# Kernel optimization log

Hardware: AMD Instinct MI355X
Metric: run time of the kernel (lower is better)

The kernel has to match this reference:

```python
import jax, jax.numpy as jnp
import numpy as np

B, T, C = 4, 2048, 1024
H = 16
D = C // H  # head_dim = 64


def setup_inputs() -> dict:
    key = jax.random.key(0)
    k1, k2, k3 = jax.random.split(key, 3)
    x = jax.random.normal(k1, (B, T, C), dtype=jnp.float32)
    w_qkv = jax.random.normal(k2, (3 * C, C), dtype=jnp.float32) * (1.0 / np.sqrt(C))
    w_proj = jax.random.normal(k3, (C, C), dtype=jnp.float32) * (1.0 / np.sqrt(C))
    return {"x": x, "w_qkv": w_qkv, "w_proj": w_proj}


def reference(x, w_qkv, w_proj):
    Bx, Tx, Cx = x.shape
    qkv = jnp.einsum('btc,fc->btf', x, w_qkv)  # [B,T,3C]
    q, k, v = jnp.split(qkv, 3, axis=-1)
    # [B,H,T,D]
    q = q.reshape(Bx, Tx, H, D).transpose(0, 2, 1, 3)
    k = k.reshape(Bx, Tx, H, D).transpose(0, 2, 1, 3)
    v = v.reshape(Bx, Tx, H, D).transpose(0, 2, 1, 3)
    scale = 1.0 / np.sqrt(D)
    scores = jnp.einsum('bhqd,bhkd->bhqk', q, k) * scale
    causal = jnp.tril(jnp.ones((Tx, Tx), dtype=bool))
    scores = jnp.where(causal, scores, jnp.finfo(scores.dtype).min)
    attn = jax.nn.softmax(scores, axis=-1)
    out = jnp.einsum('bhqk,bhkd->bhqd', attn, v)  # [B,H,T,D]
    out = out.transpose(0, 2, 1, 3).reshape(Bx, Tx, Cx)
    return jnp.einsum('btc,oc->bto', out, w_proj)
```

## Files before the change

### kernel.cpp

```cpp
#include <hip/hip_runtime.h>
#include <hip/hip_bf16.h>
#include <stdint.h>

#define Bx 4
#define Tx 2048
#define Cx 1024
#define Hx 16
#define Dx 64
#define Mx (Bx*Tx)

typedef __bf16 bf16x8 __attribute__((ext_vector_type(8)));
typedef float f32x4 __attribute__((ext_vector_type(4)));
typedef unsigned short u16x8 __attribute__((ext_vector_type(8)));

__device__ __forceinline__ unsigned short f2bf(float f) {
  union { float f; unsigned u; } v; v.f = f;
  unsigned r = v.u + 0x7fffu + ((v.u >> 16) & 1u);
  return (unsigned short)(r >> 16);
}

__device__ __forceinline__ unsigned cvt_pk_bf16(float a, float b) {
  unsigned r;
  asm("v_cvt_pk_bf16_f32 %0, %1, %2" : "=v"(r) : "v"(a), "v"(b));
  return r;
}

__global__ void cvt3_kernel(const float* __restrict__ x, const float* __restrict__ wq,
                            const float* __restrict__ wp,
                            unsigned short* __restrict__ xb, unsigned short* __restrict__ wqb,
                            unsigned short* __restrict__ wpb) {
  const int n1 = Bx * Tx * Cx;
  const int n2 = 3 * Cx * Cx;
  int idx = (blockIdx.x * blockDim.x + threadIdx.x) << 3;
  const float* src; unsigned short* dst; int off;
  if (idx < n1)            { src = x;  dst = xb;  off = idx; }
  else if (idx < n1 + n2)  { src = wq; dst = wqb; off = idx - n1; }
  else                     { src = wp; dst = wpb; off = idx - n1 - n2; }
  const float4* p = (const float4*)(src + off);
  float4 a = p[0], b = p[1];
  u16x8 o;
  o[0] = f2bf(a.x); o[1] = f2bf(a.y); o[2] = f2bf(a.z); o[3] = f2bf(a.w);
  o[4] = f2bf(b.x); o[5] = f2bf(b.y); o[6] = f2bf(b.z); o[7] = f2bf(b.w);
  *(u16x8*)(dst + off) = o;
}

#define GLOAD_LDS16(g, l) \
  __builtin_amdgcn_global_load_lds((const __attribute__((address_space(1))) void*)(g), \
                                   (__attribute__((address_space(3))) void*)(l), 16, 0, 0)

template<int OUT_F32>
__global__ __launch_bounds__(512, 1) void gemm8p(const unsigned short* __restrict__ A,
                                                 const unsigned short* __restrict__ Bm,
                                                 void* __restrict__ Cv,
                                                 int M, int N, int K)
{
  __shared__ unsigned short As[3][256 * 64];
  __shared__ unsigned short Bs[3][128 * 64];
  const int tid = threadIdx.x;
  const int wave = tid >> 6, lane = tid & 63;
  const int l15 = lane & 15, l4 = lane >> 4;
  const int wm = wave >> 1, wn = wave & 1;
  const int NB = N >> 7;
  const int cpx = (int)gridDim.x >> 3;
  const int bid = (int)blockIdx.x;
  const int swz = (bid & 7) * cpx + (bid >> 3);
  const int bx = swz % NB, by = swz / NB;
  const int mBase = by << 8, nBase = bx << 7;

  const int srow   = tid >> 3;
  const int schunk = (tid & 7) ^ (srow & 7);
  const unsigned short* aSrc = A  + (size_t)(mBase + srow) * K + (schunk << 3);
  const unsigned short* bSrc = Bm + (size_t)(nBase + srow) * K + (schunk << 3);
  const int dstOff = wave << 9;

  f32x4 acc[4][4];
  #pragma unroll
  for (int i = 0; i < 4; ++i)
    #pragma unroll
    for (int j = 0; j < 4; ++j) { acc[i][j][0]=0.f; acc[i][j][1]=0.f; acc[i][j][2]=0.f; acc[i][j][3]=0.f; }

  const int NT = K >> 6;
  const int s7 = l15 & 7;

#define STG_A(k0, dst, j)  GLOAD_LDS16(aSrc + (size_t)(64*(j))*K + (k0), (dst) + 4096*(j) + dstOff)
#define STG_B(k0, dst, j)  GLOAD_LDS16(bSrc + (size_t)(64*(j))*K + (k0), (dst) + 4096*(j) + dstOff)

  STG_A(0, As[0], 0); STG_A(0, As[0], 1); STG_A(0, As[0], 2); STG_A(0, As[0], 3);
  STG_B(0, Bs[0], 0); STG_B(0, Bs[0], 1);
  STG_A(64, As[1], 0); STG_A(64, As[1], 1); STG_A(64, As[1], 2); STG_A(64, As[1], 3);
  STG_B(64, Bs[1], 0); STG_B(64, Bs[1], 1);

  int bufR = 0;
  for (int t = 0; t < NT; ++t) {
    if (t + 1 < NT) asm volatile("s_waitcnt vmcnt(6)" ::: "memory");
    else            asm volatile("s_waitcnt vmcnt(0)" ::: "memory");
    __builtin_amdgcn_s_barrier();
    asm volatile("" ::: "memory");

    const unsigned short* curA = As[bufR];
    const unsigned short* curB = Bs[bufR];
    int bufS = bufR + 2; if (bufS >= 3) bufS -= 3;
    unsigned short* sA = As[bufS];
    unsigned short* sB = Bs[bufS];
    const bool doStage = (t + 2 < NT);
    const int k2 = (t + 2) << 6;

    if (doStage) { STG_A(k2, sA, 0); STG_A(k2, sA, 1); STG_A(k2, sA, 2); }
    {
      const int ch = l4 ^ s7;
      bf16x8 af[4], bfr[4];
      #pragma unroll
      for (int mi = 0; mi < 4; ++mi)
        af[mi]  = *(const bf16x8*)&curA[((wm << 6) + (mi << 4) + l15) * 64 + (ch << 3)];
      #pragma unroll
      for (int nj = 0; nj < 4; ++nj)
        bfr[nj] = *(const bf16x8*)&curB[((wn << 6) + (nj << 4) + l15) * 64 + (ch << 3)];
      __builtin_amdgcn_s_setprio(1);
      #pragma unroll
      for (int mi = 0; mi < 4; ++mi)
        #pragma unroll
        for (int nj = 0; nj < 4; ++nj)
          acc[mi][nj] = __builtin_amdgcn_mfma_f32_16x16x32_bf16(af[mi], bfr[nj], acc[mi][nj], 0, 0, 0);
      __builtin_amdgcn_s_setprio(0);
    }
    if (doStage) { STG_A(k2, sA, 3); STG_B(k2, sB, 0); STG_B(k2, sB, 1); }
    {
      const int ch = (4 | l4) ^ s7;
      bf16x8 af[4], bfr[4];
      #pragma unroll
      for (int mi = 0; mi < 4; ++mi)
        af[mi]  = *(const bf16x8*)&curA[((wm << 6) + (mi << 4) + l15) * 64 + (ch << 3)];
      #pragma unroll
      for (int nj = 0; nj < 4; ++nj)
        bfr[nj] = *(const bf16x8*)&curB[((wn << 6) + (nj << 4) + l15) * 64 + (ch << 3)];
      __builtin_amdgcn_s_setprio(1);
      #pragma unroll
      for (int mi = 0; mi < 4; ++mi)
        #pragma unroll
        for (int nj = 0; nj < 4; ++nj)
          acc[mi][nj] = __builtin_amdgcn_mfma_f32_16x16x32_bf16(af[mi], bfr[nj], acc[mi][nj], 0, 0, 0);
      __builtin_amdgcn_s_setprio(0);
    }
    asm volatile("" ::: "memory");
    bufR = (bufR == 2) ? 0 : bufR + 1;
  }
#undef STG_A
#undef STG_B

  #pragma unroll
  for (int mi = 0; mi < 4; ++mi)
    #pragma unroll
    for (int nj = 0; nj < 4; ++nj) {
      const int row = mBase + (wm << 6) + (mi << 4) + (l4 << 2);
      const int col = nBase + (wn << 6) + (nj << 4) + l15;
      #pragma unroll
      for (int r = 0; r < 4; ++r) {
        float v = acc[mi][nj][r];
        if (OUT_F32) ((float*)Cv)[(size_t)(row + r) * N + col] = v;
        else ((unsigned short*)Cv)[(size_t)(row + r) * N + col] = f2bf(v);
      }
    }
}

__global__ void vtrans_kernel(const unsigned short* __restrict__ qkv, unsigned short* __restrict__ vt) {
  const int bh = blockIdx.y;
  const int b = bh >> 4, h = bh & 15;
  const int t0 = blockIdx.x << 6;
  __shared__ unsigned short tile[64][65];
  const int tid = threadIdx.x;
  const unsigned short* src = qkv + (size_t)b * Tx * 3072 + 2048 + h * 64;
  for (int e = tid; e < 4096; e += 256) {
    int r = e >> 6, c = e & 63;
    tile[c][r] = src[(size_t)(t0 + r) * 3072 + c];
  }
  __syncthreads();
  unsigned short* dst = vt + (size_t)bh * 64 * Tx + t0;
  for (int e = tid; e < 4096; e += 256) {
    int d = e >> 6, tt = e & 63;
    dst[(size_t)d * Tx + tt] = tile[d][tt];
  }
}

__device__ __forceinline__ void compute_half(
    const unsigned short* __restrict__ Ks, const unsigned short* __restrict__ Vs,
    unsigned short* __restrict__ Plw,
    bf16x8 aq0, bf16x8 aq1, float& m_run, float& rs, f32x4* oacc,
    int qrow0, int kv0, bool diag, int l15, int l4)
{
  const float SC = 0.125f * 1.44269504f;
  f32x4 s[4];
  #pragma unroll
  for (int nt = 0; nt < 4; ++nt) { s[nt][0]=0.f; s[nt][1]=0.f; s[nt][2]=0.f; s[nt][3]=0.f; }
  #pragma unroll
  for (int nt = 0; nt < 4; ++nt) {
    const int r = (nt << 4) + l15, sz = r & 7;
    bf16x8 bk0 = *(const bf16x8*)&Ks[r * 64 + ((l4 ^ sz) << 3)];
    bf16x8 bk1 = *(const bf16x8*)&Ks[r * 64 + (((l4 + 4) ^ sz) << 3)];
    s[nt] = __builtin_amdgcn_mfma_f32_16x16x32_bf16(bk0, aq0, s[nt], 0, 0, 0);
    s[nt] = __builtin_amdgcn_mfma_f32_16x16x32_bf16(bk1, aq1, s[nt], 0, 0, 0);
  }
  if (diag) {
    const int q = qrow0 + l15;
    #pragma unroll
    for (int nt = 0; nt < 4; ++nt) {
      const int kvb = kv0 + (nt << 4) + (l4 << 2);
      #pragma unroll
      for (int r = 0; r < 4; ++r)
        if (kvb + r > q) s[nt][r] = -3.0e38f;
    }
  }
  float pm = fmaxf(fmaxf(fmaxf(s[0][0],s[0][1]),fmaxf(s[0][2],s[0][3])),
                   fmaxf(fmaxf(s[1][0],s[1][1]),fmaxf(s[1][2],s[1][3])));
  pm = fmaxf(pm, fmaxf(fmaxf(fmaxf(s[2][0],s[2][1]),fmaxf(s[2][2],s[2][3])),
                       fmaxf(fmaxf(s[3][0],s[3][1]),fmaxf(s[3][2],s[3][3]))));
  const float DEFER = 44.36142f;
  if (!__all(pm <= m_run + DEFER)) {
    pm = fmaxf(pm, __shfl_xor(pm, 16));
    pm = fmaxf(pm, __shfl_xor(pm, 32));
    const float mnew = fmaxf(m_run, pm);
    const float corr = exp2f((m_run - mnew) * SC);
    rs *= corr;
    float corrT[4];
    #pragma unroll
    for (int r = 0; r < 4; ++r) corrT[r] = __shfl(corr, (l4 << 2) + r);
    #pragma unroll
    for (int nt = 0; nt < 4; ++nt)
      #pragma unroll
      for (int r = 0; r < 4; ++r) oacc[nt][r] *= corrT[r];
    m_run = mnew;
  }
  const float msc = m_run * SC;
  float lsum = 0.f;
  #pragma unroll
  for (int nt = 0; nt < 4; ++nt)
    #pragma unroll
    for (int r = 0; r < 4; ++r) {
      float p = exp2f(__builtin_fmaf(s[nt][r], SC, -msc));
      s[nt][r] = p;
      lsum += p;
    }
  rs += lsum;
  #pragma unroll
  for (int nt = 0; nt < 4; ++nt) {
    uint2 u;
    u.x = cvt_pk_bf16(s[nt][0], s[nt][1]);
    u.y = cvt_pk_bf16(s[nt][2], s[nt][3]);
    *(uint2*)&Plw[l15 * 72 + (nt << 4) + (l4 << 2)] = u;
  }
  asm volatile("s_waitcnt lgkmcnt(0)" ::: "memory");
  __builtin_amdgcn_sched_barrier(0);
  bf16x8 ap0 = *(const bf16x8*)&Plw[l15 * 72 + (l4 << 3)];
  bf16x8 ap1 = *(const bf16x8*)&Plw[l15 * 72 + 32 + (l4 << 3)];
  #pragma unroll
  for (int nt = 0; nt < 4; ++nt) {
    const int r = (nt << 4) + l15, vz = r & 7;
    bf16x8 bv0 = *(const bf16x8*)&Vs[r * 64 + ((l4 ^ vz) << 3)];
    bf16x8 bv1 = *(const bf16x8*)&Vs[r * 64 + (((l4 + 4) ^ vz) << 3)];
    oacc[nt] = __builtin_amdgcn_mfma_f32_16x16x32_bf16(ap0, bv0, oacc[nt], 0, 0, 0);
    oacc[nt] = __builtin_amdgcn_mfma_f32_16x16x32_bf16(ap1, bv1, oacc[nt], 0, 0, 0);
  }
}

__global__ __launch_bounds__(256, 4) void attn_kernel(const unsigned short* __restrict__ qkv,
                                                      const unsigned short* __restrict__ vt,
                                                      unsigned short* __restrict__ aout)
{
  const int id = blockIdx.x;
  const int xcd = id & 7, sblk = id >> 3;
  const int xblk = sblk & 15;
  const int bh = (xcd << 3) + (sblk >> 4);
  const int b = bh >> 4, h = bh & 15;
  const int wave = threadIdx.x >> 6, lane = threadIdx.x & 63;
  const int l15 = lane & 15, l4 = lane >> 4;
  const int qi0 = (xblk << 2) + wave;

  const unsigned short* qp = qkv + (size_t)b * Tx * 3072 + h * 64;
  const unsigned short* kp = qp + 1024;
  const unsigned short* vp = vt + (size_t)bh * 64 * Tx;
  unsigned short* op = aout + (size_t)b * Tx * 1024 + h * 64;

  __shared__ unsigned short Ks[64 * 64];
  __shared__ unsigned short Vs[64 * 64];
  __shared__ unsigned short Pl[4][2][16 * 72];

  const int qiA = qi0, qiB = 127 - qi0;
  const int qrA = qiA << 4, qrB = qiB << 4;
  const int lastA = xblk, lastB = 31 - xblk;

  bf16x8 aqA0 = *(const bf16x8*)&qp[(size_t)(qrA + l15) * 3072 + (l4 << 3)];
  bf16x8 aqA1 = *(const bf16x8*)&qp[(size_t)(qrA + l15) * 3072 + 32 + (l4 << 3)];
  bf16x8 aqB0 = *(const bf16x8*)&qp[(size_t)(qrB + l15) * 3072 + (l4 << 3)];
  bf16x8 aqB1 = *(const bf16x8*)&qp[(size_t)(qrB + l15) * 3072 + 32 + (l4 << 3)];

  float mA = 0.f, rsA = 0.f, mB = 0.f, rsB = 0.f;
  f32x4 oA[4], oB[4];
  #pragma unroll
  for (int nt = 0; nt < 4; ++nt) {
    oA[nt][0]=0.f; oA[nt][1]=0.f; oA[nt][2]=0.f; oA[nt][3]=0.f;
    oB[nt][0]=0.f; oB[nt][1]=0.f; oB[nt][2]=0.f; oB[nt][3]=0.f;
  }

  const int srw = lane >> 3;
  const int sj  = (lane & 7) ^ srw;

  for (int kvt = 0; kvt <= lastB; ++kvt) {
    const int kv0 = kvt << 6;
    {
      const int c0 = wave << 1, c1 = c0 + 1;
      const int r0 = (c0 << 3) + srw, r1 = (c1 << 3) + srw;
      GLOAD_LDS16(kp + (size_t)(kv0 + r0) * 3072 + (sj << 3), Ks + (c0 << 9));
      GLOAD_LDS16(kp + (size_t)(kv0 + r1) * 3072 + (sj << 3), Ks + (c1 << 9));
      GLOAD_LDS16(vp + (size_t)r0 * 2048 + kv0 + (sj << 3),   Vs + (c0 << 9));
      GLOAD_LDS16(vp + (size_t)r1 * 2048 + kv0 + (sj << 3),   Vs + (c1 << 9));
    }
    __syncthreads();

    compute_half(Ks, Vs, Pl[wave][1], aqB0, aqB1, mB, rsB, oB, qrB, kv0, kvt == lastB, l15, l4);
    if (kvt <= lastA)
      compute_half(Ks, Vs, Pl[wave][0], aqA0, aqA1, mA, rsA, oA, qrA, kv0, kvt == lastA, l15, l4);

    __syncthreads();
  }

  rsA += __shfl_xor(rsA, 16); rsA += __shfl_xor(rsA, 32);
  rsB += __shfl_xor(rsB, 16); rsB += __shfl_xor(rsB, 32);
  #pragma unroll
  for (int r = 0; r < 4; ++r) {
    const float invA = 1.0f / __shfl(rsA, (l4 << 2) + r);
    const float invB = 1.0f / __shfl(rsB, (l4 << 2) + r);
    #pragma unroll
    for (int nt = 0; nt < 4; ++nt) {
      op[(size_t)(qrA + (l4 << 2) + r) * 1024 + (nt << 4) + l15] = f2bf(oA[nt][r] * invA);
      op[(size_t)(qrB + (l4 << 2) + r) * 1024 + (nt << 4) + l15] = f2bf(oB[nt][r] * invB);
    }
  }
}

extern "C" void kernel_launch(void* const* d_in, const int* in_sizes, int n_in,
                              void* d_out, int out_size, void* d_ws, size_t ws_size,
                              hipStream_t stream) {
  const float* x     = (const float*)d_in[0];
  const float* wqkv  = (const float*)d_in[1];
  const float* wproj = (const float*)d_in[2];

  char* ws = (char*)d_ws;
  unsigned short* qkvb = (unsigned short*)(ws);
  unsigned short* vtb  = (unsigned short*)(ws + 50331648);
  unsigned short* xb   = (unsigned short*)(ws + 50331648 + 16777216);
  unsigned short* wqb  = (unsigned short*)(ws + 50331648 + 16777216 + 16777216);
  unsigned short* wpb  = (unsigned short*)(ws + 50331648 + 16777216 + 16777216 + 6291456);
  unsigned short* aob  = xb;

  cvt3_kernel<<<6144, 256, 0, stream>>>(x, wqkv, wproj, xb, wqb, wpb);

  gemm8p<0><<<dim3(768), 512, 0, stream>>>(xb, wqb, qkvb, Mx, 3072, 1024);
  vtrans_kernel<<<dim3(32, 64), 256, 0, stream>>>(qkvb, vtb);
  attn_kernel<<<1024, 256, 0, stream>>>(qkvb, vtb, aob);
  gemm8p<1><<<dim3(256), 512, 0, stream>>>(aob, wpb, d_out, Mx, 1024, 1024);
}
```

Before: 275.2 us.

## Fuse V transpose into QKV GEMM epilogue and double-buffer attention K/V tiles

The QKV GEMM epilogue now writes the V columns straight into the transposed [B,H,D,T] layout with packed 4-element stores, so the separate vtrans kernel and its extra read and write of V are gone. The attention kernel double-buffers its K/V shared-memory tiles: it issues the next tile's global-to-LDS loads before computing the current one and waits with vmcnt, and the two per-wave P buffers are merged into one. The occupancy hint drops from 4 to 3 blocks per CU to make room for the larger LDS footprint. The max reduction is also rewritten as a linear chain, which may allow fused 3-input max instructions. The risks are lower occupancy and that the V columns are no longer written to qkv, which is fine because attention reads V only from the transposed buffer.

New measurement: 277.5 us. Within noise of the previous version (+0.8%).

```diff
diff --git a/kernel.cpp b/kernel.cpp
--- a/kernel.cpp
+++ b/kernel.cpp
@@ -12,6 +12,7 @@
 typedef __bf16 bf16x8 __attribute__((ext_vector_type(8)));
 typedef float f32x4 __attribute__((ext_vector_type(4)));
 typedef unsigned short u16x8 __attribute__((ext_vector_type(8)));
+typedef unsigned short u16x4 __attribute__((ext_vector_type(4)));
 
 __device__ __forceinline__ unsigned short f2bf(float f) {
   union { float f; unsigned u; } v; v.f = f;
@@ -52,6 +53,7 @@
 __global__ __launch_bounds__(512, 1) void gemm8p(const unsigned short* __restrict__ A,
                                                  const unsigned short* __restrict__ Bm,
                                                  void* __restrict__ Cv,
+                                                 unsigned short* __restrict__ vt,
                                                  int M, int N, int K)
 {
   __shared__ unsigned short As[3][256 * 64];
@@ -147,37 +149,36 @@
 #undef STG_A
 #undef STG_B
 
-  #pragma unroll
-  for (int mi = 0; mi < 4; ++mi)
-    #pragma unroll
-    for (int nj = 0; nj < 4; ++nj) {
-      const int row = mBase + (wm << 6) + (mi << 4) + (l4 << 2);
-      const int col = nBase + (wn << 6) + (nj << 4) + l15;
-      #pragma unroll
-      for (int r = 0; r < 4; ++r) {
-        float v = acc[mi][nj][r];
-        if (OUT_F32) ((float*)Cv)[(size_t)(row + r) * N + col] = v;
-        else ((unsigned short*)Cv)[(size_t)(row + r) * N + col] = f2bf(v);
+  if (!OUT_F32 && nBase >= 2048) {
+    const int hh = ((nBase - 2048) >> 6) | wn;
+    const int bb = mBase >> 11;
+    unsigned short* vbase = vt + ((size_t)((bb << 4) + hh) << 17);
+    const int tb = (mBase & 2047) + (wm << 6) + (l4 << 2);
+    #pragma unroll
+    for (int mi = 0; mi < 4; ++mi) {
+      #pragma unroll
+      for (int nj = 0; nj < 4; ++nj) {
+        const int d = (nj << 4) + l15;
+        u16x4 pk;
+        pk[0] = f2bf(acc[mi][nj][0]); pk[1] = f2bf(acc[mi][nj][1]);
+        pk[2] = f2bf(acc[mi][nj][2]); pk[3] = f2bf(acc[mi][nj][3]);
+        *(u16x4*)&vbase[((size_t)d << 11) + tb + (mi << 4)] = pk;
       }
     }
-}
-
-__global__ void vtrans_kernel(const unsigned short* __restrict__ qkv, unsigned short* __restrict__ vt) {
-  const int bh = blockIdx.y;
-  const int b = bh >> 4, h = bh & 15;
-  const int t0 = blockIdx.x << 6;
-  __shared__ unsigned short tile[64][65];
-  const int tid = threadIdx.x;
-  const unsigned short* src = qkv + (size_t)b * Tx * 3072 + 2048 + h * 64;
-  for (int e = tid; e < 4096; e += 256) {
-    int r = e >> 6, c = e & 63;
-    tile[c][r] = src[(size_t)(t0 + r) * 3072 + c];
-  }
-  __syncthreads();
-  unsigned short* dst = vt + (size_t)bh * 64 * Tx + t0;
-  for (int e = tid; e < 4096; e += 256) {
-    int d = e >> 6, tt = e & 63;
-    dst[(size_t)d * Tx + tt] = tile[d][tt];
+  } else {
+    #pragma unroll
+    for (int mi = 0; mi < 4; ++mi)
+      #pragma unroll
+      for (int nj = 0; nj < 4; ++nj) {
+        const int row = mBase + (wm << 6) + (mi << 4) + (l4 << 2);
+        const int col = nBase + (wn << 6) + (nj << 4) + l15;
+        #pragma unroll
+        for (int r = 0; r < 4; ++r) {
+          float v = acc[mi][nj][r];
+          if (OUT_F32) ((float*)Cv)[(size_t)(row + r) * N + col] = v;
+          else ((unsigned short*)Cv)[(size_t)(row + r) * N + col] = f2bf(v);
+        }
+      }
   }
 }
 
@@ -209,10 +210,14 @@
         if (kvb + r > q) s[nt][r] = -3.0e38f;
     }
   }
-  float pm = fmaxf(fmaxf(fmaxf(s[0][0],s[0][1]),fmaxf(s[0][2],s[0][3])),
-                   fmaxf(fmaxf(s[1][0],s[1][1]),fmaxf(s[1][2],s[1][3])));
-  pm = fmaxf(pm, fmaxf(fmaxf(fmaxf(s[2][0],s[2][1]),fmaxf(s[2][2],s[2][3])),
-                       fmaxf(fmaxf(s[3][0],s[3][1]),fmaxf(s[3][2],s[3][3]))));
+  float pm = fmaxf(fmaxf(s[0][0], s[0][1]), s[0][2]);
+  pm = fmaxf(fmaxf(pm, s[0][3]), s[1][0]);
+  pm = fmaxf(fmaxf(pm, s[1][1]), s[1][2]);
+  pm = fmaxf(fmaxf(pm, s[1][3]), s[2][0]);
+  pm = fmaxf(fmaxf(pm, s[2][1]), s[2][2]);
+  pm = fmaxf(fmaxf(pm, s[2][3]), s[3][0]);
+  pm = fmaxf(fmaxf(pm, s[3][1]), s[3][2]);
+  pm = fmaxf(pm, s[3][3]);
   const float DEFER = 44.36142f;
   if (!__all(pm <= m_run + DEFER)) {
     pm = fmaxf(pm, __shfl_xor(pm, 16));
@@ -261,7 +266,7 @@
   }
 }
 
-__global__ __launch_bounds__(256, 4) void attn_kernel(const unsigned short* __restrict__ qkv,
+__global__ __launch_bounds__(256, 3) void attn_kernel(const unsigned short* __restrict__ qkv,
                                                       const unsigned short* __restrict__ vt,
                                                       unsigned short* __restrict__ aout)
 {
@@ -279,9 +284,9 @@
   const unsigned short* vp = vt + (size_t)bh * 64 * Tx;
   unsigned short* op = aout + (size_t)b * Tx * 1024 + h * 64;
 
-  __shared__ unsigned short Ks[64 * 64];
-  __shared__ unsigned short Vs[64 * 64];
-  __shared__ unsigned short Pl[4][2][16 * 72];
+  __shared__ unsigned short Ks[2][64 * 64];
+  __shared__ unsigned short Vs[2][64 * 64];
+  __shared__ unsigned short Pl[4][16 * 72];
 
   const int qiA = qi0, qiB = 127 - qi0;
   const int qrA = qiA << 4, qrB = qiB << 4;
@@ -302,25 +307,37 @@
 
   const int srw = lane >> 3;
   const int sj  = (lane & 7) ^ srw;
-
+  const int c0 = wave << 1, c1 = c0 + 1;
+  const int r0 = (c0 << 3) + srw, r1 = (c1 << 3) + srw;
+
+#define STAGE_KV(kvt, buf) do { \
+    const int kv_ = (kvt) << 6; \
+    GLOAD_LDS16(kp + (size_t)(kv_ + r0) * 3072 + (sj << 3), Ks[buf] + (c0 << 9)); \
+    GLOAD_LDS16(kp + (size_t)(kv_ + r1) * 3072 + (sj << 3), Ks[buf] + (c1 << 9)); \
+    GLOAD_LDS16(vp + (size_t)r0 * 2048 + kv_ + (sj << 3),   Vs[buf] + (c0 << 9)); \
+    GLOAD_LDS16(vp + (size_t)r1 * 2048 + kv_ + (sj << 3),   Vs[buf] + (c1 << 9)); \
+  } while (0)
+
+  STAGE_KV(0, 0);
   for (int kvt = 0; kvt <= lastB; ++kvt) {
-    const int kv0 = kvt << 6;
-    {
-      const int c0 = wave << 1, c1 = c0 + 1;
-      const int r0 = (c0 << 3) + srw, r1 = (c1 << 3) + srw;
-      GLOAD_LDS16(kp + (size_t)(kv0 + r0) * 3072 + (sj << 3), Ks + (c0 << 9));
-      GLOAD_LDS16(kp + (size_t)(kv0 + r1) * 3072 + (sj << 3), Ks + (c1 << 9));
-      GLOAD_LDS16(vp + (size_t)r0 * 2048 + kv0 + (sj << 3),   Vs + (c0 << 9));
-      GLOAD_LDS16(vp + (size_t)r1 * 2048 + kv0 + (sj << 3),   Vs + (c1 << 9));
-    }
-    __syncthreads();
-
-    compute_half(Ks, Vs, Pl[wave][1], aqB0, aqB1, mB, rsB, oB, qrB, kv0, kvt == lastB, l15, l4);
+    const int buf = kvt & 1;
+    if (kvt < lastB) {
+      STAGE_KV(kvt + 1, buf ^ 1);
+      asm volatile("s_waitcnt vmcnt(4)" ::: "memory");
+    } else {
+      asm volatile("s_waitcnt vmcnt(0)" ::: "memory");
+    }
+    __builtin_amdgcn_s_barrier();
+    asm volatile("" ::: "memory");
+
+    compute_half(Ks[buf], Vs[buf], Pl[wave], aqB0, aqB1, mB, rsB, oB, qrB, kvt << 6, kvt == lastB, l15, l4);
     if (kvt <= lastA)
-      compute_half(Ks, Vs, Pl[wave][0], aqA0, aqA1, mA, rsA, oA, qrA, kv0, kvt == lastA, l15, l4);
-
-    __syncthreads();
-  }
+      compute_half(Ks[buf], Vs[buf], Pl[wave], aqA0, aqA1, mA, rsA, oA, qrA, kvt << 6, kvt == lastA, l15, l4);
+
+    asm volatile("" ::: "memory");
+    __builtin_amdgcn_s_barrier();
+  }
+#undef STAGE_KV
 
   rsA += __shfl_xor(rsA, 16); rsA += __shfl_xor(rsA, 32);
   rsB += __shfl_xor(rsB, 16); rsB += __shfl_xor(rsB, 32);
@@ -353,8 +370,7 @@
 
   cvt3_kernel<<<6144, 256, 0, stream>>>(x, wqkv, wproj, xb, wqb, wpb);
 
-  gemm8p<0><<<dim3(768), 512, 0, stream>>>(xb, wqb, qkvb, Mx, 3072, 1024);
-  vtrans_kernel<<<dim3(32, 64), 256, 0, stream>>>(qkvb, vtb);
+  gemm8p<0><<<dim3(768), 512, 0, stream>>>(xb, wqb, qkvb, vtb, Mx, 3072, 1024);
   attn_kernel<<<1024, 256, 0, stream>>>(qkvb, vtb, aob);
-  gemm8p<1><<<dim3(256), 512, 0, stream>>>(aob, wpb, d_out, Mx, 1024, 1024);
-}
+  gemm8p<1><<<dim3(256), 512, 0, stream>>>(aob, wpb, d_out, nullptr, Mx, 1024, 1024);
+}
```
